# Optimization experiments

Hardware: AMD Instinct MI355X
Metric: run time of the kernel (lower is better)

The kernel has to match this reference:

```python
import jax, jax.numpy as jnp
import numpy as np

B, T, C, H = 4, 2048, 512, 8
D = C // H  # head dim = 64

def setup_inputs() -> dict:
    key = jax.random.key(0)
    ks = jax.random.split(key, 6)
    x = jax.random.normal(ks[0], (B, T, C), dtype=jnp.float32)
    # per-batch graph adjacency mask: True = attend, False = masked
    adj_matrix = jax.random.bernoulli(ks[1], 0.5, (B, T, T))
    # ensure self-edges so no row is fully masked
    adj_matrix = adj_matrix | jnp.eye(T, dtype=bool)[None]
    s = 0.02
    w_qkv = jax.random.normal(ks[2], (C, 3 * C), dtype=jnp.float32) * s
    b_qkv = jnp.zeros((3 * C,), dtype=jnp.float32)
    w_proj = jax.random.normal(ks[3], (C, C), dtype=jnp.float32) * s
    b_proj = jnp.zeros((C,), dtype=jnp.float32)
    return {"x": x, "adj_matrix": adj_matrix, "w_qkv": w_qkv, "b_qkv": b_qkv,
            "w_proj": w_proj, "b_proj": b_proj}

def reference(x, adj_matrix, w_qkv, b_qkv, w_proj, b_proj):
    Bx, Tx, Cx = x.shape
    qkv = x @ w_qkv + b_qkv                       # [B,T,3C]
    q, k, v = jnp.split(qkv, 3, axis=-1)
    def heads(t):
        return t.reshape(Bx, Tx, H, D).transpose(0, 2, 1, 3)  # [B,H,T,D]
    q, k, v = heads(q), heads(k), heads(v)
    scale = 1.0 / jnp.sqrt(jnp.asarray(D, dtype=x.dtype))
    scores = jnp.einsum('bhtd,bhsd->bhts', q, k) * scale      # [B,H,T,T]
    neg = jnp.finfo(scores.dtype).min
    scores = jnp.where(adj_matrix[:, None, :, :], scores, neg)
    attn = jax.nn.softmax(scores, axis=-1)
    y = jnp.einsum('bhts,bhsd->bhtd', attn, v)                # [B,H,T,D]
    y = y.transpose(0, 2, 1, 3).reshape(Bx, Tx, Cx)           # [B,T,C]
    return y @ w_proj + b_proj
```

## Files before the change

kernel.cpp:

```cpp
#include <hip/hip_runtime.h>
#include <stdint.h>

typedef __attribute__((ext_vector_type(8))) __bf16 bf16x8;
typedef __attribute__((ext_vector_type(4))) __bf16 bf16x4;
typedef __attribute__((ext_vector_type(2))) __bf16 bf16x2;
typedef __attribute__((ext_vector_type(4))) float f32x4;
typedef __attribute__((ext_vector_type(16))) float f32x16;
typedef __attribute__((ext_vector_type(4))) unsigned u32x4;
typedef __attribute__((ext_vector_type(2))) int i32x2;

__device__ __forceinline__ unsigned short f2bf(float f) {
  unsigned u = __float_as_uint(f);
  u += 0x7FFFu + ((u >> 16) & 1u);
  return (unsigned short)(u >> 16);
}

__device__ __forceinline__ float exp2fast(float x) {
#if __has_builtin(__builtin_amdgcn_exp2f)
  return __builtin_amdgcn_exp2f(x);
#else
  return __expf(x * 0.6931471805599453f);
#endif
}

__device__ __forceinline__ void pl32swap(unsigned &a, unsigned &b) {
#if __has_builtin(__builtin_amdgcn_permlane32_swap)
  i32x2 r = __builtin_amdgcn_permlane32_swap((int)a, (int)b, false, false);
  a = (unsigned)r[0]; b = (unsigned)r[1];
#else
  asm volatile("v_permlane32_swap_b32 %0, %1" : "+v"(a), "+v"(b));
#endif
}

__device__ __forceinline__ void gload16(const unsigned short* src, unsigned short* ldsdst) {
  __builtin_amdgcn_global_load_lds(
      (const __attribute__((address_space(1))) unsigned int*)src,
      (__attribute__((address_space(3))) unsigned int*)ldsdst, 16, 0, 0);
}

__device__ __forceinline__ void stage8(const unsigned short* gbase, long long strideElems,
                                       unsigned short* ldsTile, int rowBase) {
  const int lane = threadIdx.x & 63;
  const int r = rowBase + (lane >> 3);
  const int oct = (lane & 7) ^ (r & 7);
  gload16(gbase + (long long)r * strideElems + oct * 8, ldsTile + rowBase * 64);
}


__global__ __launch_bounds__(256) void prep(const float* __restrict__ x,
                                            unsigned short* __restrict__ xb,
                                            const float* __restrict__ wq,
                                            unsigned short* __restrict__ wqt,
                                            const float* __restrict__ wp,
                                            unsigned short* __restrict__ wpt,
                                            const int* __restrict__ adj,
                                            unsigned long long* __restrict__ mb) {
  int blk = blockIdx.x;
  if (blk < 16384) {
    int tid = blk * 256 + threadIdx.x;
    int4 v = ((const int4*)adj)[tid];
    unsigned n = (v.x != 0 ? 1u : 0u) | (v.y != 0 ? 2u : 0u) |
                 (v.z != 0 ? 4u : 0u) | (v.w != 0 ? 8u : 0u);
    unsigned long long part = (unsigned long long)n << ((threadIdx.x & 15) * 4);
    part |= __shfl_xor(part, 1);
    part |= __shfl_xor(part, 2);
    part |= __shfl_xor(part, 4);
    part |= __shfl_xor(part, 8);
    if ((threadIdx.x & 15) == 0) mb[tid >> 4] = part;
    return;
  }
  blk -= 16384;
  if (blk < 4096) {
    int i = (blk * 256 + threadIdx.x) * 4;
    float4 v = *(const float4*)(x + i);
    ushort4 o;
    o.x = f2bf(v.x); o.y = f2bf(v.y); o.z = f2bf(v.z); o.w = f2bf(v.w);
    *(ushort4*)(xb + i) = o;
    return;
  }
  blk -= 4096;
  const float* w; unsigned short* wt; int N; int bx, by;
  if (blk < 768) { w = wq; wt = wqt; N = 1536; bx = blk & 15; by = blk >> 4; }
  else { blk -= 768; w = wp; wt = wpt; N = 512; bx = blk & 15; by = blk >> 4; }
  __shared__ float tile[32][33];
  int k0 = bx * 32, n0 = by * 32;
  int tx = threadIdx.x & 31, ty = threadIdx.x >> 5;
#pragma unroll
  for (int i = 0; i < 4; i++)
    tile[ty + i * 8][tx] = w[(long long)(k0 + ty + i * 8) * N + n0 + tx];
  __syncthreads();
#pragma unroll
  for (int i = 0; i < 4; i++)
    wt[(long long)(n0 + ty + i * 8) * 512 + k0 + tx] = f2bf(tile[tx][ty + i * 8]);
}


__device__ __forceinline__ void gemm_core(const unsigned short* __restrict__ A,
                                          const unsigned short* __restrict__ Wt,
                                          unsigned short (*Al)[128 * 64],
                                          unsigned short (*Bl)[128 * 64],
                                          int m0, int n0, f32x4 acc[4][4]) {
  const int lane = threadIdx.x & 63;
  const int wid = threadIdx.x >> 6;
  const int c = lane & 15, g = lane >> 4;
  const int wm = wid >> 1, wn = wid & 1;
  const unsigned short* Ab = A + (long long)m0 * 512;
  const unsigned short* Bb = Wt + (long long)n0 * 512;

#pragma unroll
  for (int i = 0; i < 4; i++) stage8(Ab, 512, Al[0], wid * 32 + i * 8);
#pragma unroll
  for (int i = 0; i < 4; i++) stage8(Bb, 512, Bl[0], wid * 32 + i * 8);
  asm volatile("s_waitcnt vmcnt(0)" ::: "memory");
  __syncthreads();

  int cur = 0;
  for (int k0 = 0; k0 < 512; k0 += 64) {
    if (k0 + 64 < 512) {
#pragma unroll
      for (int i = 0; i < 4; i++) stage8(Ab + k0 + 64, 512, Al[cur ^ 1], wid * 32 + i * 8);
#pragma unroll
      for (int i = 0; i < 4; i++) stage8(Bb + k0 + 64, 512, Bl[cur ^ 1], wid * 32 + i * 8);
    }
#pragma unroll
    for (int kk = 0; kk < 2; kk++) {
      bf16x8 af[4], bfr[4];
#pragma unroll
      for (int mi = 0; mi < 4; mi++) {
        int row = wm * 64 + mi * 16 + c;
        af[mi] = *(const bf16x8*)&Al[cur][row * 64 + (((kk << 2) | g) ^ (row & 7)) * 8];
      }
#pragma unroll
      for (int ni = 0; ni < 4; ni++) {
        int row = wn * 64 + ni * 16 + c;
        bfr[ni] = *(const bf16x8*)&Bl[cur][row * 64 + (((kk << 2) | g) ^ (row & 7)) * 8];
      }
#pragma unroll
      for (int mi = 0; mi < 4; mi++)
#pragma unroll
        for (int ni = 0; ni < 4; ni++)
          acc[mi][ni] = __builtin_amdgcn_mfma_f32_16x16x32_bf16(af[mi], bfr[ni], acc[mi][ni], 0, 0, 0);
    }
    asm volatile("s_waitcnt vmcnt(0)" ::: "memory");
    __syncthreads();
    cur ^= 1;
  }
}

__global__ __launch_bounds__(256) void gemm_qkv(const unsigned short* __restrict__ xb,
                                                const unsigned short* __restrict__ wqt,
                                                const float* __restrict__ bqkv,
                                                unsigned short* __restrict__ qb,
                                                unsigned short* __restrict__ kb,
                                                unsigned short* __restrict__ vtb) {
  __shared__ __align__(16) unsigned short Al[2][128 * 64];
  __shared__ __align__(16) unsigned short Bl[2][128 * 64];
  f32x4 acc[4][4] = {};
  int m0 = blockIdx.x * 128, n0 = blockIdx.y * 128;
  gemm_core(xb, wqt, Al, Bl, m0, n0, acc);
  const int lane = threadIdx.x & 63;
  const int wid = threadIdx.x >> 6;
  const int c = lane & 15, g = lane >> 4;
  const int wm = wid >> 1, wn = wid & 1;
#pragma unroll
  for (int ni = 0; ni < 4; ni++) {
    int n = n0 + wn * 64 + ni * 16 + c;
    float bv = bqkv[n];
    int which = n >> 9;
    int h = (n & 511) >> 6, d = n & 63;
#pragma unroll
    for (int mi = 0; mi < 4; mi++) {
      int mbase = m0 + wm * 64 + mi * 16 + g * 4;
#pragma unroll
      for (int j = 0; j < 4; j++) {
        int m = mbase + j;
        int b = m >> 11, t = m & 2047;
        int bh = b * 8 + h;
        float v = acc[mi][ni][j] + bv;
        if (which == 0)      qb[(bh * 2048 + t) * 64 + d] = f2bf(v * 0.18033688011112042f);
        else if (which == 1) kb[(bh * 2048 + t) * 64 + d] = f2bf(v);
        else                 vtb[(bh * 64 + d) * 2048 + t] = f2bf(v);
      }
    }
  }
}

__global__ __launch_bounds__(256) void gemm_proj(const unsigned short* __restrict__ yb,
                                                 const unsigned short* __restrict__ wpt,
                                                 const float* __restrict__ bproj,
                                                 float* __restrict__ out) {
  __shared__ __align__(16) unsigned short Al[2][128 * 64];
  __shared__ __align__(16) unsigned short Bl[2][128 * 64];
  f32x4 acc[4][4] = {};
  int m0 = blockIdx.x * 128, n0 = blockIdx.y * 128;
  gemm_core(yb, wpt, Al, Bl, m0, n0, acc);
  const int lane = threadIdx.x & 63;
  const int wid = threadIdx.x >> 6;
  const int c = lane & 15, g = lane >> 4;
  const int wm = wid >> 1, wn = wid & 1;
#pragma unroll
  for (int ni = 0; ni < 4; ni++) {
    int n = n0 + wn * 64 + ni * 16 + c;
    float bv = bproj[n];
#pragma unroll
    for (int mi = 0; mi < 4; mi++) {
      int mbase = m0 + wm * 64 + mi * 16 + g * 4;
#pragma unroll
      for (int j = 0; j < 4; j++)
        out[(long long)(mbase + j) * 512 + n] = acc[mi][ni][j] + bv;
    }
  }
}

__global__ __launch_bounds__(128) void attn(const unsigned short* __restrict__ qb,
                                            const unsigned short* __restrict__ kb,
                                            const unsigned short* __restrict__ vtb,
                                            const unsigned long long* __restrict__ mbits,
                                            unsigned short* __restrict__ yb) {
  __shared__ __align__(16) unsigned short Kl[2][64 * 64];
  __shared__ __align__(16) unsigned short Vl[2][64 * 64];
  const int lane = threadIdx.x & 63;
  const int w = threadIdx.x >> 6;
  const int l31 = lane & 31, h5 = lane >> 5;
  const int swz = l31 & 7;
  const int bh = blockIdx.y;
  const int b = bh >> 3, h = bh & 7;
  const int q0 = blockIdx.x * 64;
  const int qglob = q0 + w * 32 + l31;

  const unsigned short* qptr = qb + ((long long)bh * 2048 + qglob) * 64;
  bf16x8 qf[4];
#pragma unroll
  for (int cc = 0; cc < 4; cc++) qf[cc] = *(const bf16x8*)(qptr + cc * 16 + h5 * 8);

  const unsigned long long* mrow = mbits + ((long long)b * 2048 + qglob) * 32;
  const unsigned short* kbase = kb + (long long)bh * 2048 * 64;
  const unsigned short* vbase = vtb + (long long)bh * 64 * 2048;

  f32x16 accO0 = {0,0,0,0, 0,0,0,0, 0,0,0,0, 0,0,0,0};
  f32x16 accO1 = {0,0,0,0, 0,0,0,0, 0,0,0,0, 0,0,0,0};
  float lrun = 0.0f;

#pragma unroll
  for (int i = 0; i < 4; i++) stage8(kbase, 64, Kl[0], w * 32 + i * 8);
#pragma unroll
  for (int i = 0; i < 4; i++) stage8(vbase, 2048, Vl[0], w * 32 + i * 8);
  unsigned long long mw = mrow[0];
  asm volatile("s_waitcnt vmcnt(0)" ::: "memory");
  __syncthreads();

  int cur = 0;
  for (int t = 0; t < 32; ++t) {
    unsigned long long mwn = 0;
    if (t < 31) {
      int kv0 = (t + 1) * 64;
#pragma unroll
      for (int i = 0; i < 4; i++) stage8(kbase + (long long)kv0 * 64, 64, Kl[cur ^ 1], w * 32 + i * 8);
#pragma unroll
      for (int i = 0; i < 4; i++) stage8(vbase + kv0, 2048, Vl[cur ^ 1], w * 32 + i * 8);
      mwn = mrow[t + 1];
    }

    const unsigned short* Kb = &Kl[cur][0];
    const unsigned short* Vb = &Vl[cur][0];
    f32x16 st0 = {0,0,0,0, 0,0,0,0, 0,0,0,0, 0,0,0,0};
    f32x16 st1 = {0,0,0,0, 0,0,0,0, 0,0,0,0, 0,0,0,0};
    __builtin_amdgcn_s_setprio(1);
#pragma unroll
    for (int cc = 0; cc < 4; cc++) {
      int u = ((cc * 2 + h5) ^ swz) * 8;
      bf16x8 kf0 = *(const bf16x8*)&Kb[l31 * 64 + u];
      bf16x8 kf1 = *(const bf16x8*)&Kb[(32 + l31) * 64 + u];
      st0 = __builtin_amdgcn_mfma_f32_32x32x16_bf16(kf0, qf[cc], st0, 0, 0, 0);
      st1 = __builtin_amdgcn_mfma_f32_32x32x16_bf16(kf1, qf[cc], st1, 0, 0, 0);
    }
    __builtin_amdgcn_s_setprio(0);

    unsigned mh0 = ((unsigned)mw) >> (4 * h5);
    unsigned mh1 = ((unsigned)(mw >> 32)) >> (4 * h5);
    unsigned pd[2][8];
    float lsum = 0.0f;
#pragma unroll
    for (int m = 0; m < 8; m++) {
      const int r0 = 2 * m, r1 = 2 * m + 1;
      const int bi0 = (r0 & 3) + 8 * (r0 >> 2);
      const int bi1 = (r1 & 3) + 8 * (r1 >> 2);
      float p0 = ((mh0 >> bi0) & 1u) ? exp2fast(st0[r0]) : 0.0f;
      float p1 = ((mh0 >> bi1) & 1u) ? exp2fast(st0[r1]) : 0.0f;
      float p2 = ((mh1 >> bi0) & 1u) ? exp2fast(st1[r0]) : 0.0f;
      float p3 = ((mh1 >> bi1) & 1u) ? exp2fast(st1[r1]) : 0.0f;
      lsum += (p0 + p1) + (p2 + p3);
      bf16x2 v0 = {(__bf16)p0, (__bf16)p1};
      bf16x2 v1 = {(__bf16)p2, (__bf16)p3};
      pd[0][m] = __builtin_bit_cast(unsigned, v0);
      pd[1][m] = __builtin_bit_cast(unsigned, v1);
    }
    lrun += lsum;

#pragma unroll
    for (int ot = 0; ot < 2; ot++)
#pragma unroll
      for (int hc = 0; hc < 2; hc++) {
        pl32swap(pd[ot][4 * hc + 0], pd[ot][4 * hc + 2]);
        pl32swap(pd[ot][4 * hc + 1], pd[ot][4 * hc + 3]);
      }

    __builtin_amdgcn_s_setprio(1);
#pragma unroll
    for (int cc = 0; cc < 4; cc++) {
      u32x4 pu = {pd[cc >> 1][4 * (cc & 1) + 0], pd[cc >> 1][4 * (cc & 1) + 1],
                  pd[cc >> 1][4 * (cc & 1) + 2], pd[cc >> 1][4 * (cc & 1) + 3]};
      bf16x8 pf = __builtin_bit_cast(bf16x8, pu);
      int u = ((cc * 2 + h5) ^ swz) * 8;
      bf16x8 vf0 = *(const bf16x8*)&Vb[l31 * 64 + u];
      bf16x8 vf1 = *(const bf16x8*)&Vb[(32 + l31) * 64 + u];
      accO0 = __builtin_amdgcn_mfma_f32_32x32x16_bf16(vf0, pf, accO0, 0, 0, 0);
      accO1 = __builtin_amdgcn_mfma_f32_32x32x16_bf16(vf1, pf, accO1, 0, 0, 0);
    }
    __builtin_amdgcn_s_setprio(0);

    asm volatile("s_waitcnt vmcnt(0)" ::: "memory");
    __syncthreads();
    cur ^= 1;
    mw = mwn;
  }

  float linv = 1.0f / (lrun + __shfl_xor(lrun, 32));
  unsigned short* yrow = yb + ((long long)(b * 2048 + qglob)) * 512 + h * 64;
#pragma unroll
  for (int m = 0; m < 4; m++) {
    int d0 = 8 * m + 4 * h5;
    bf16x4 o0 = {(__bf16)(accO0[4 * m + 0] * linv), (__bf16)(accO0[4 * m + 1] * linv),
                 (__bf16)(accO0[4 * m + 2] * linv), (__bf16)(accO0[4 * m + 3] * linv)};
    bf16x4 o1 = {(__bf16)(accO1[4 * m + 0] * linv), (__bf16)(accO1[4 * m + 1] * linv),
                 (__bf16)(accO1[4 * m + 2] * linv), (__bf16)(accO1[4 * m + 3] * linv)};
    *(bf16x4*)&yrow[d0] = o0;
    *(bf16x4*)&yrow[32 + d0] = o1;
  }
}


extern "C" void kernel_launch(void* const* d_in, const int* in_sizes, int n_in,
                              void* d_out, int out_size, void* d_ws, size_t ws_size,
                              hipStream_t stream) {
  const float* x      = (const float*)d_in[0];
  const int*   adj    = (const int*)d_in[1];
  const float* w_qkv  = (const float*)d_in[2];
  const float* b_qkv  = (const float*)d_in[3];
  const float* w_proj = (const float*)d_in[4];
  const float* b_proj = (const float*)d_in[5];
  float* out = (float*)d_out;

  char* ws = (char*)d_ws;
  unsigned short* xb  = (unsigned short*)(ws);
  unsigned short* qb  = (unsigned short*)(ws + 8388608);
  unsigned short* kbf = (unsigned short*)(ws + 16777216);
  unsigned short* vtb = (unsigned short*)(ws + 25165824);
  unsigned short* wqt = (unsigned short*)(ws + 33554432);
  unsigned short* wpt = (unsigned short*)(ws + 35127296);
  unsigned long long* mb = (unsigned long long*)(ws + 35651584);
  unsigned short* yb = xb;

  prep<<<dim3(21504), dim3(256), 0, stream>>>(x, xb, w_qkv, wqt, w_proj, wpt, adj, mb);
  gemm_qkv<<<dim3(64, 12), dim3(256), 0, stream>>>(xb, wqt, b_qkv, qb, kbf, vtb);
  attn<<<dim3(32, 32), dim3(128), 0, stream>>>(qb, kbf, vtb, mb, yb);
  gemm_proj<<<dim3(64, 4), dim3(256), 0, stream>>>(yb, wpt, b_proj, out);
}
```

Measured before the change: 132.4 us.

## Split attention KV range in two blocks and combine partials in separate kernel

Attention blocks now each cover half of the key/value sequence, doubling the grid from 1024 to 2048 blocks. Each writes unnormalized fp32 partial outputs and row sums, and a new combine kernel adds the two halves, normalizes and writes bf16. The mask is applied by seeding the score accumulator with 0 or -1e30 before the MFMA instead of selecting after exp. The LDS swizzle also changes to mix in row bits 3-4 to reduce bank conflicts. The cost is extra fp32 global traffic and one more kernel launch.

```diff
diff --git a/kernel.cpp b/kernel.cpp
--- a/kernel.cpp
+++ b/kernel.cpp
@@ -32,6 +32,8 @@
 #endif
 }
 
+__device__ __forceinline__ int swz8(int r) { return (r & 7) ^ ((r >> 3) & 3); }
+
 __device__ __forceinline__ void gload16(const unsigned short* src, unsigned short* ldsdst) {
   __builtin_amdgcn_global_load_lds(
       (const __attribute__((address_space(1))) unsigned int*)src,
@@ -42,7 +44,7 @@
                                        unsigned short* ldsTile, int rowBase) {
   const int lane = threadIdx.x & 63;
   const int r = rowBase + (lane >> 3);
-  const int oct = (lane & 7) ^ (r & 7);
+  const int oct = (lane & 7) ^ swz8(r);
   gload16(gbase + (long long)r * strideElems + oct * 8, ldsTile + rowBase * 64);
 }
 
@@ -128,12 +130,12 @@
 #pragma unroll
       for (int mi = 0; mi < 4; mi++) {
         int row = wm * 64 + mi * 16 + c;
-        af[mi] = *(const bf16x8*)&Al[cur][row * 64 + (((kk << 2) | g) ^ (row & 7)) * 8];
+        af[mi] = *(const bf16x8*)&Al[cur][row * 64 + (((kk << 2) | g) ^ swz8(row)) * 8];
       }
 #pragma unroll
       for (int ni = 0; ni < 4; ni++) {
         int row = wn * 64 + ni * 16 + c;
-        bfr[ni] = *(const bf16x8*)&Bl[cur][row * 64 + (((kk << 2) | g) ^ (row & 7)) * 8];
+        bfr[ni] = *(const bf16x8*)&Bl[cur][row * 64 + (((kk << 2) | g) ^ swz8(row)) * 8];
       }
 #pragma unroll
       for (int mi = 0; mi < 4; mi++)
@@ -216,16 +218,21 @@
                                             const unsigned short* __restrict__ kb,
                                             const unsigned short* __restrict__ vtb,
                                             const unsigned long long* __restrict__ mbits,
-                                            unsigned short* __restrict__ yb) {
+                                            float* __restrict__ opart,
+                                            float* __restrict__ lpart) {
   __shared__ __align__(16) unsigned short Kl[2][64 * 64];
   __shared__ __align__(16) unsigned short Vl[2][64 * 64];
   const int lane = threadIdx.x & 63;
   const int w = threadIdx.x >> 6;
   const int l31 = lane & 31, h5 = lane >> 5;
-  const int swz = l31 & 7;
-  const int bh = blockIdx.y;
+  const int sA = swz8(l31);
+  const int bid = blockIdx.x;
+  const int bh = bid & 31;
+  const int tmp = bid >> 5;
+  const int q0 = (tmp & 31) * 64;
+  const int z = tmp >> 5;
+  const int kvbase = z * 1024;
   const int b = bh >> 3, h = bh & 7;
-  const int q0 = blockIdx.x * 64;
   const int qglob = q0 + w * 32 + l31;
 
   const unsigned short* qptr = qb + ((long long)bh * 2048 + qglob) * 64;
@@ -233,7 +240,7 @@
 #pragma unroll
   for (int cc = 0; cc < 4; cc++) qf[cc] = *(const bf16x8*)(qptr + cc * 16 + h5 * 8);
 
-  const unsigned long long* mrow = mbits + ((long long)b * 2048 + qglob) * 32;
+  const unsigned long long* mrow = mbits + ((long long)b * 2048 + qglob) * 32 + z * 16;
   const unsigned short* kbase = kb + (long long)bh * 2048 * 64;
   const unsigned short* vbase = vtb + (long long)bh * 64 * 2048;
 
@@ -242,18 +249,18 @@
   float lrun = 0.0f;
 
 #pragma unroll
-  for (int i = 0; i < 4; i++) stage8(kbase, 64, Kl[0], w * 32 + i * 8);
-#pragma unroll
-  for (int i = 0; i < 4; i++) stage8(vbase, 2048, Vl[0], w * 32 + i * 8);
+  for (int i = 0; i < 4; i++) stage8(kbase + (long long)kvbase * 64, 64, Kl[0], w * 32 + i * 8);
+#pragma unroll
+  for (int i = 0; i < 4; i++) stage8(vbase + kvbase, 2048, Vl[0], w * 32 + i * 8);
   unsigned long long mw = mrow[0];
   asm volatile("s_waitcnt vmcnt(0)" ::: "memory");
   __syncthreads();
 
   int cur = 0;
-  for (int t = 0; t < 32; ++t) {
+  for (int t = 0; t < 16; ++t) {
     unsigned long long mwn = 0;
-    if (t < 31) {
-      int kv0 = (t + 1) * 64;
+    if (t < 15) {
+      int kv0 = kvbase + (t + 1) * 64;
 #pragma unroll
       for (int i = 0; i < 4; i++) stage8(kbase + (long long)kv0 * 64, 64, Kl[cur ^ 1], w * 32 + i * 8);
 #pragma unroll
@@ -261,14 +268,22 @@
       mwn = mrow[t + 1];
     }
 
+    unsigned mh0 = ((unsigned)mw) >> (4 * h5);
+    unsigned mh1 = ((unsigned)(mw >> 32)) >> (4 * h5);
+    f32x16 st0, st1;
+#pragma unroll
+    for (int r = 0; r < 16; r++) {
+      const int bi = (r & 3) + 8 * (r >> 2);
+      st0[r] = ((mh0 >> bi) & 1u) ? 0.0f : -1e30f;
+      st1[r] = ((mh1 >> bi) & 1u) ? 0.0f : -1e30f;
+    }
+
     const unsigned short* Kb = &Kl[cur][0];
     const unsigned short* Vb = &Vl[cur][0];
-    f32x16 st0 = {0,0,0,0, 0,0,0,0, 0,0,0,0, 0,0,0,0};
-    f32x16 st1 = {0,0,0,0, 0,0,0,0, 0,0,0,0, 0,0,0,0};
     __builtin_amdgcn_s_setprio(1);
 #pragma unroll
     for (int cc = 0; cc < 4; cc++) {
-      int u = ((cc * 2 + h5) ^ swz) * 8;
+      int u = ((cc * 2 + h5) ^ sA) * 8;
       bf16x8 kf0 = *(const bf16x8*)&Kb[l31 * 64 + u];
       bf16x8 kf1 = *(const bf16x8*)&Kb[(32 + l31) * 64 + u];
       st0 = __builtin_amdgcn_mfma_f32_32x32x16_bf16(kf0, qf[cc], st0, 0, 0, 0);
@@ -276,19 +291,15 @@
     }
     __builtin_amdgcn_s_setprio(0);
 
-    unsigned mh0 = ((unsigned)mw) >> (4 * h5);
-    unsigned mh1 = ((unsigned)(mw >> 32)) >> (4 * h5);
     unsigned pd[2][8];
     float lsum = 0.0f;
 #pragma unroll
     for (int m = 0; m < 8; m++) {
       const int r0 = 2 * m, r1 = 2 * m + 1;
-      const int bi0 = (r0 & 3) + 8 * (r0 >> 2);
-      const int bi1 = (r1 & 3) + 8 * (r1 >> 2);
-      float p0 = ((mh0 >> bi0) & 1u) ? exp2fast(st0[r0]) : 0.0f;
-      float p1 = ((mh0 >> bi1) & 1u) ? exp2fast(st0[r1]) : 0.0f;
-      float p2 = ((mh1 >> bi0) & 1u) ? exp2fast(st1[r0]) : 0.0f;
-      float p3 = ((mh1 >> bi1) & 1u) ? exp2fast(st1[r1]) : 0.0f;
+      float p0 = exp2fast(st0[r0]);
+      float p1 = exp2fast(st0[r1]);
+      float p2 = exp2fast(st1[r0]);
+      float p3 = exp2fast(st1[r1]);
       lsum += (p0 + p1) + (p2 + p3);
       bf16x2 v0 = {(__bf16)p0, (__bf16)p1};
       bf16x2 v1 = {(__bf16)p2, (__bf16)p3};
@@ -311,7 +322,7 @@
       u32x4 pu = {pd[cc >> 1][4 * (cc & 1) + 0], pd[cc >> 1][4 * (cc & 1) + 1],
                   pd[cc >> 1][4 * (cc & 1) + 2], pd[cc >> 1][4 * (cc & 1) + 3]};
       bf16x8 pf = __builtin_bit_cast(bf16x8, pu);
-      int u = ((cc * 2 + h5) ^ swz) * 8;
+      int u = ((cc * 2 + h5) ^ sA) * 8;
       bf16x8 vf0 = *(const bf16x8*)&Vb[l31 * 64 + u];
       bf16x8 vf1 = *(const bf16x8*)&Vb[(32 + l31) * 64 + u];
       accO0 = __builtin_amdgcn_mfma_f32_32x32x16_bf16(vf0, pf, accO0, 0, 0, 0);
@@ -325,18 +336,35 @@
     mw = mwn;
   }
 
-  float linv = 1.0f / (lrun + __shfl_xor(lrun, 32));
-  unsigned short* yrow = yb + ((long long)(b * 2048 + qglob)) * 512 + h * 64;
+  float* op = opart + ((((long long)z * 32 + bh) * 2048 + qglob) * 64);
 #pragma unroll
   for (int m = 0; m < 4; m++) {
     int d0 = 8 * m + 4 * h5;
-    bf16x4 o0 = {(__bf16)(accO0[4 * m + 0] * linv), (__bf16)(accO0[4 * m + 1] * linv),
-                 (__bf16)(accO0[4 * m + 2] * linv), (__bf16)(accO0[4 * m + 3] * linv)};
-    bf16x4 o1 = {(__bf16)(accO1[4 * m + 0] * linv), (__bf16)(accO1[4 * m + 1] * linv),
-                 (__bf16)(accO1[4 * m + 2] * linv), (__bf16)(accO1[4 * m + 3] * linv)};
-    *(bf16x4*)&yrow[d0] = o0;
-    *(bf16x4*)&yrow[32 + d0] = o1;
-  }
+    f32x4 o0 = {accO0[4 * m + 0], accO0[4 * m + 1], accO0[4 * m + 2], accO0[4 * m + 3]};
+    f32x4 o1 = {accO1[4 * m + 0], accO1[4 * m + 1], accO1[4 * m + 2], accO1[4 * m + 3]};
+    *(f32x4*)&op[d0] = o0;
+    *(f32x4*)&op[32 + d0] = o1;
+  }
+  float ltot = lrun + __shfl_xor(lrun, 32);
+  if (h5 == 0) lpart[(long long)z * 65536 + bh * 2048 + qglob] = ltot;
+}
+
+__global__ __launch_bounds__(256) void combine(const float* __restrict__ p0,
+                                               const float* __restrict__ p1,
+                                               const float* __restrict__ l0,
+                                               const float* __restrict__ l1,
+                                               unsigned short* __restrict__ yb) {
+  int idx = blockIdx.x * 256 + threadIdx.x;
+  int bhq = idx >> 4, d4 = idx & 15;
+  float4 a = ((const float4*)p0)[idx];
+  float4 c = ((const float4*)p1)[idx];
+  float linv = 1.0f / (l0[bhq] + l1[bhq]);
+  int bh = bhq >> 11, q = bhq & 2047;
+  int b = bh >> 3, h = bh & 7;
+  unsigned short* dst = yb + ((long long)(b * 2048 + q)) * 512 + h * 64 + d4 * 4;
+  bf16x4 o = {(__bf16)((a.x + c.x) * linv), (__bf16)((a.y + c.y) * linv),
+              (__bf16)((a.z + c.z) * linv), (__bf16)((a.w + c.w) * linv)};
+  *(bf16x4*)dst = o;
 }
 
 
@@ -359,10 +387,14 @@
   unsigned short* wqt = (unsigned short*)(ws + 33554432);
   unsigned short* wpt = (unsigned short*)(ws + 35127296);
   unsigned long long* mb = (unsigned long long*)(ws + 35651584);
+  float* opart = (float*)(ws + 37748736);
+  float* lpart = (float*)(ws + 71303168);
   unsigned short* yb = xb;
 
   prep<<<dim3(21504), dim3(256), 0, stream>>>(x, xb, w_qkv, wqt, w_proj, wpt, adj, mb);
   gemm_qkv<<<dim3(64, 12), dim3(256), 0, stream>>>(xb, wqt, b_qkv, qb, kbf, vtb);
-  attn<<<dim3(32, 32), dim3(128), 0, stream>>>(qb, kbf, vtb, mb, yb);
+  attn<<<dim3(2048), dim3(128), 0, stream>>>(qb, kbf, vtb, mb, opart, lpart);
+  combine<<<dim3(4096), dim3(256), 0, stream>>>(opart, opart + 16777216 / 4,
+                                                lpart, lpart + 65536, yb);
   gemm_proj<<<dim3(64, 4), dim3(256), 0, stream>>>(yb, wpt, b_proj, out);
 }
```

Measured after the change: 143.2 us. +8.2%, slower.

## Widen attention blocks, preload mask as additive bias, and change LDS swizzle

Applied to the files above, without the earlier changes.

The attention kernel now runs 4 waves per block covering 128 queries, so each staged K/V tile is shared by twice as many waves and each wave issues half the staging loads. The mask is turned into an additive 0/-1e30 bias through a small LDS lookup table and used as the MFMA accumulator's initial value, which removes the per-element select before exp2. The LDS swizzle now also XORs in row bits 3-4, aimed at reducing bank conflicts in both the GEMM and attention tiles. The grid is flattened to 1D with the head index in the low bits to improve K/V locality across neighbouring blocks. The trade-off is fewer, larger blocks and extra LDS reads for the bias table.

```diff
diff --git a/kernel.cpp b/kernel.cpp
--- a/kernel.cpp
+++ b/kernel.cpp
@@ -32,6 +32,8 @@
 #endif
 }
 
+__device__ __forceinline__ int swz8(int r) { return (r & 7) ^ ((r >> 3) & 3); }
+
 __device__ __forceinline__ void gload16(const unsigned short* src, unsigned short* ldsdst) {
   __builtin_amdgcn_global_load_lds(
       (const __attribute__((address_space(1))) unsigned int*)src,
@@ -42,7 +44,7 @@
                                        unsigned short* ldsTile, int rowBase) {
   const int lane = threadIdx.x & 63;
   const int r = rowBase + (lane >> 3);
-  const int oct = (lane & 7) ^ (r & 7);
+  const int oct = (lane & 7) ^ swz8(r);
   gload16(gbase + (long long)r * strideElems + oct * 8, ldsTile + rowBase * 64);
 }
 
@@ -128,12 +130,12 @@
 #pragma unroll
       for (int mi = 0; mi < 4; mi++) {
         int row = wm * 64 + mi * 16 + c;
-        af[mi] = *(const bf16x8*)&Al[cur][row * 64 + (((kk << 2) | g) ^ (row & 7)) * 8];
+        af[mi] = *(const bf16x8*)&Al[cur][row * 64 + (((kk << 2) | g) ^ swz8(row)) * 8];
       }
 #pragma unroll
       for (int ni = 0; ni < 4; ni++) {
         int row = wn * 64 + ni * 16 + c;
-        bfr[ni] = *(const bf16x8*)&Bl[cur][row * 64 + (((kk << 2) | g) ^ (row & 7)) * 8];
+        bfr[ni] = *(const bf16x8*)&Bl[cur][row * 64 + (((kk << 2) | g) ^ swz8(row)) * 8];
       }
 #pragma unroll
       for (int mi = 0; mi < 4; mi++)
@@ -212,21 +214,29 @@
   }
 }
 
-__global__ __launch_bounds__(128) void attn(const unsigned short* __restrict__ qb,
+__global__ __launch_bounds__(256) void attn(const unsigned short* __restrict__ qb,
                                             const unsigned short* __restrict__ kb,
                                             const unsigned short* __restrict__ vtb,
                                             const unsigned long long* __restrict__ mbits,
                                             unsigned short* __restrict__ yb) {
   __shared__ __align__(16) unsigned short Kl[2][64 * 64];
   __shared__ __align__(16) unsigned short Vl[2][64 * 64];
+  __shared__ __align__(16) float lut4[16][4];
   const int lane = threadIdx.x & 63;
   const int w = threadIdx.x >> 6;
   const int l31 = lane & 31, h5 = lane >> 5;
-  const int swz = l31 & 7;
-  const int bh = blockIdx.y;
+  const int sA = swz8(l31);
+  const int bid = blockIdx.x;
+  const int bh = bid & 31;
+  const int q0 = (bid >> 5) * 128;
   const int b = bh >> 3, h = bh & 7;
-  const int q0 = blockIdx.x * 64;
   const int qglob = q0 + w * 32 + l31;
+
+  if (threadIdx.x < 16) {
+    int n = threadIdx.x;
+#pragma unroll
+    for (int j = 0; j < 4; j++) lut4[n][j] = ((n >> j) & 1) ? 0.0f : -1e30f;
+  }
 
   const unsigned short* qptr = qb + ((long long)bh * 2048 + qglob) * 64;
   bf16x8 qf[4];
@@ -241,10 +251,10 @@
   f32x16 accO1 = {0,0,0,0, 0,0,0,0, 0,0,0,0, 0,0,0,0};
   float lrun = 0.0f;
 
-#pragma unroll
-  for (int i = 0; i < 4; i++) stage8(kbase, 64, Kl[0], w * 32 + i * 8);
-#pragma unroll
-  for (int i = 0; i < 4; i++) stage8(vbase, 2048, Vl[0], w * 32 + i * 8);
+  stage8(kbase, 64, Kl[0], w * 16);
+  stage8(kbase, 64, Kl[0], w * 16 + 8);
+  stage8(vbase, 2048, Vl[0], w * 16);
+  stage8(vbase, 2048, Vl[0], w * 16 + 8);
   unsigned long long mw = mrow[0];
   asm volatile("s_waitcnt vmcnt(0)" ::: "memory");
   __syncthreads();
@@ -254,21 +264,29 @@
     unsigned long long mwn = 0;
     if (t < 31) {
       int kv0 = (t + 1) * 64;
-#pragma unroll
-      for (int i = 0; i < 4; i++) stage8(kbase + (long long)kv0 * 64, 64, Kl[cur ^ 1], w * 32 + i * 8);
-#pragma unroll
-      for (int i = 0; i < 4; i++) stage8(vbase + kv0, 2048, Vl[cur ^ 1], w * 32 + i * 8);
+      stage8(kbase + (long long)kv0 * 64, 64, Kl[cur ^ 1], w * 16);
+      stage8(kbase + (long long)kv0 * 64, 64, Kl[cur ^ 1], w * 16 + 8);
+      stage8(vbase + kv0, 2048, Vl[cur ^ 1], w * 16);
+      stage8(vbase + kv0, 2048, Vl[cur ^ 1], w * 16 + 8);
       mwn = mrow[t + 1];
+    }
+
+    unsigned lo = (unsigned)mw, hi = (unsigned)(mw >> 32);
+    f32x16 st0, st1;
+#pragma unroll
+    for (int j = 0; j < 4; j++) {
+      f32x4 s0 = *(const f32x4*)lut4[(lo >> (8 * j + 4 * h5)) & 0xF];
+      f32x4 s1 = *(const f32x4*)lut4[(hi >> (8 * j + 4 * h5)) & 0xF];
+#pragma unroll
+      for (int i = 0; i < 4; i++) { st0[4 * j + i] = s0[i]; st1[4 * j + i] = s1[i]; }
     }
 
     const unsigned short* Kb = &Kl[cur][0];
     const unsigned short* Vb = &Vl[cur][0];
-    f32x16 st0 = {0,0,0,0, 0,0,0,0, 0,0,0,0, 0,0,0,0};
-    f32x16 st1 = {0,0,0,0, 0,0,0,0, 0,0,0,0, 0,0,0,0};
     __builtin_amdgcn_s_setprio(1);
 #pragma unroll
     for (int cc = 0; cc < 4; cc++) {
-      int u = ((cc * 2 + h5) ^ swz) * 8;
+      int u = ((cc * 2 + h5) ^ sA) * 8;
       bf16x8 kf0 = *(const bf16x8*)&Kb[l31 * 64 + u];
       bf16x8 kf1 = *(const bf16x8*)&Kb[(32 + l31) * 64 + u];
       st0 = __builtin_amdgcn_mfma_f32_32x32x16_bf16(kf0, qf[cc], st0, 0, 0, 0);
@@ -276,19 +294,15 @@
     }
     __builtin_amdgcn_s_setprio(0);
 
-    unsigned mh0 = ((unsigned)mw) >> (4 * h5);
-    unsigned mh1 = ((unsigned)(mw >> 32)) >> (4 * h5);
     unsigned pd[2][8];
     float lsum = 0.0f;
 #pragma unroll
     for (int m = 0; m < 8; m++) {
       const int r0 = 2 * m, r1 = 2 * m + 1;
-      const int bi0 = (r0 & 3) + 8 * (r0 >> 2);
-      const int bi1 = (r1 & 3) + 8 * (r1 >> 2);
-      float p0 = ((mh0 >> bi0) & 1u) ? exp2fast(st0[r0]) : 0.0f;
-      float p1 = ((mh0 >> bi1) & 1u) ? exp2fast(st0[r1]) : 0.0f;
-      float p2 = ((mh1 >> bi0) & 1u) ? exp2fast(st1[r0]) : 0.0f;
-      float p3 = ((mh1 >> bi1) & 1u) ? exp2fast(st1[r1]) : 0.0f;
+      float p0 = exp2fast(st0[r0]);
+      float p1 = exp2fast(st0[r1]);
+      float p2 = exp2fast(st1[r0]);
+      float p3 = exp2fast(st1[r1]);
       lsum += (p0 + p1) + (p2 + p3);
       bf16x2 v0 = {(__bf16)p0, (__bf16)p1};
       bf16x2 v1 = {(__bf16)p2, (__bf16)p3};
@@ -311,7 +325,7 @@
       u32x4 pu = {pd[cc >> 1][4 * (cc & 1) + 0], pd[cc >> 1][4 * (cc & 1) + 1],
                   pd[cc >> 1][4 * (cc & 1) + 2], pd[cc >> 1][4 * (cc & 1) + 3]};
       bf16x8 pf = __builtin_bit_cast(bf16x8, pu);
-      int u = ((cc * 2 + h5) ^ swz) * 8;
+      int u = ((cc * 2 + h5) ^ sA) * 8;
       bf16x8 vf0 = *(const bf16x8*)&Vb[l31 * 64 + u];
       bf16x8 vf1 = *(const bf16x8*)&Vb[(32 + l31) * 64 + u];
       accO0 = __builtin_amdgcn_mfma_f32_32x32x16_bf16(vf0, pf, accO0, 0, 0, 0);
@@ -363,6 +377,6 @@
 
   prep<<<dim3(21504), dim3(256), 0, stream>>>(x, xb, w_qkv, wqt, w_proj, wpt, adj, mb);
   gemm_qkv<<<dim3(64, 12), dim3(256), 0, stream>>>(xb, wqt, b_qkv, qb, kbf, vtb);
-  attn<<<dim3(32, 32), dim3(128), 0, stream>>>(qb, kbf, vtb, mb, yb);
+  attn<<<dim3(512), dim3(256), 0, stream>>>(qb, kbf, vtb, mb, yb);
   gemm_proj<<<dim3(64, 4), dim3(256), 0, stream>>>(yb, wpt, b_proj, out);
 }
```

New measurement: 118.9 us. -10.2%, faster.
